# Kernel optimization log

Measured on AMD Instinct MI355X. Metric: run time of the kernel, lower is better.

The kernel has to match this reference:

```python
import jax, jax.numpy as jnp
import numpy as np

B, S, D, H = 4, 2048, 1024, 16
DH = D // H  # dim per head

def setup_inputs() -> dict:
    key = jax.random.key(0)
    ks = jax.random.split(key, 12)
    sc = 1.0 / np.sqrt(D)
    inp = {
        "key": jax.random.normal(ks[0], (B, S, D), jnp.float32),
        "value": jax.random.normal(ks[1], (B, S, D), jnp.float32),
        "query": jax.random.normal(ks[2], (B, S, D), jnp.float32),
        "mask": jax.random.randint(ks[3], (B, S, S), 0, 2).astype(bool),
        "Wq": jax.random.normal(ks[4], (D, D), jnp.float32) * sc,
        "bq": jnp.zeros((D,), jnp.float32),
        "Wk": jax.random.normal(ks[5], (D, D), jnp.float32) * sc,
        "bk": jnp.zeros((D,), jnp.float32),
        "Wv": jax.random.normal(ks[6], (D, D), jnp.float32) * sc,
        "bv": jnp.zeros((D,), jnp.float32),
        "Wo": jax.random.normal(ks[7], (D, D), jnp.float32) * sc,
        "bo": jnp.zeros((D,), jnp.float32),
    }
    return inp

def _shape(x, b):
    # [b, len, D] -> [b, H, len, DH]
    return x.reshape(b, -1, H, DH).transpose(0, 2, 1, 3)

def reference(key, value, query, mask, Wq, bq, Wk, bk, Wv, bv, Wo, bo):
    b = key.shape[0]
    q = _shape(query @ Wq.T + bq, b) / jnp.sqrt(jnp.asarray(DH, query.dtype))
    k = _shape(key @ Wk.T + bk, b)
    v = _shape(value @ Wv.T + bv, b)
    # scores: [b, H, q_len, k_len]
    scores = jnp.einsum("bhqd,bhkd->bhqk", q, k)
    scores = jnp.where(mask[:, None, :, :], jnp.asarray(-1e18, scores.dtype), scores)
    attn = jax.nn.softmax(scores, axis=-1)  # dropout is identity in eval mode
    ctx = jnp.einsum("bhqk,bhkd->bhqd", attn, v)
    ctx = ctx.transpose(0, 2, 1, 3).reshape(b, -1, H * DH)
    return ctx @ Wo.T + bo
```

## Files before the change

kernel.cpp:

```cpp
#include <hip/hip_runtime.h>

#define BB  4
#define SS  2048
#define DD  1024
#define HH  16
#define DHH 64
#define LOG2E 1.44269504088896340736f

typedef __attribute__((ext_vector_type(8)))  _Float16 half8;
typedef __attribute__((ext_vector_type(4)))  _Float16 half4;
typedef __attribute__((ext_vector_type(2)))  float    f32x2;
typedef __attribute__((ext_vector_type(4)))  float    f32x4;
typedef __attribute__((ext_vector_type(8)))  float    f32x8;
typedef __attribute__((ext_vector_type(16))) float    f32x16;
typedef __attribute__((ext_vector_type(4)))  unsigned int uint4v;

#if __has_builtin(__builtin_amdgcn_exp2f)
#define EXP2(x) __builtin_amdgcn_exp2f(x)
#else
#define EXP2(x) exp2f(x)
#endif

__device__ __forceinline__ void gload_lds16(const void* g, void* l) {
  __builtin_amdgcn_global_load_lds(
      (const __attribute__((address_space(1))) unsigned int*)g,
      (__attribute__((address_space(3))) unsigned int*)l, 16, 0, 0);
}

__device__ __forceinline__ void plswap(unsigned int& x, unsigned int& y) {
  auto r = __builtin_amdgcn_permlane32_swap(x, y, false, false);
  x = r[0]; y = r[1];
}
__device__ __forceinline__ float xhalf_sum(float v) {
  unsigned int x = __builtin_bit_cast(unsigned int, v), y = x;
  plswap(x, y);
  return __builtin_bit_cast(float, x) + __builtin_bit_cast(float, y);
}

__device__ __forceinline__ float tree16(f32x16 t) {
  f32x8 u = __builtin_shufflevector(t, t, 0, 1, 2, 3, 4, 5, 6, 7) +
            __builtin_shufflevector(t, t, 8, 9, 10, 11, 12, 13, 14, 15);
  f32x4 v = __builtin_shufflevector(u, u, 0, 1, 2, 3) +
            __builtin_shufflevector(u, u, 4, 5, 6, 7);
  f32x2 w2 = __builtin_shufflevector(v, v, 0, 1) + __builtin_shufflevector(v, v, 2, 3);
  return w2[0] + w2[1];
}

__global__ __launch_bounds__(256) void cvt_f32_f16(
    const float* __restrict__ in, _Float16* __restrict__ out, int n4) {
  int i = blockIdx.x * 256 + threadIdx.x;
  if (i >= n4) return;
  float4 a = reinterpret_cast<const float4*>(in)[i];
  half4 h;
  h[0] = (_Float16)a.x; h[1] = (_Float16)a.y;
  h[2] = (_Float16)a.z; h[3] = (_Float16)a.w;
  reinterpret_cast<half4*>(out)[i] = h;
}

__global__ __launch_bounds__(256) void cvt_in3(
    const float* __restrict__ s0, const float* __restrict__ s1,
    const float* __restrict__ s2,
    _Float16* __restrict__ d0, _Float16* __restrict__ d1,
    _Float16* __restrict__ d2, int n4) {
  int i = blockIdx.x * 256 + threadIdx.x;
  if (i >= n4) return;
  const float* s; _Float16* d;
  switch (blockIdx.y) {
    case 0: s = s0; d = d0; break;
    case 1: s = s1; d = d1; break;
    default: s = s2; d = d2; break;
  }
  float4 a = reinterpret_cast<const float4*>(s)[i];
  half4 h;
  h[0] = (_Float16)a.x; h[1] = (_Float16)a.y;
  h[2] = (_Float16)a.z; h[3] = (_Float16)a.w;
  reinterpret_cast<half4*>(d)[i] = h;
}

__global__ __launch_bounds__(256) void cvt_w4(
    const float* __restrict__ s0, const float* __restrict__ s1,
    const float* __restrict__ s2, const float* __restrict__ s3,
    _Float16* __restrict__ d0, _Float16* __restrict__ d1,
    _Float16* __restrict__ d2, _Float16* __restrict__ d3, int n4) {
  int i = blockIdx.x * 256 + threadIdx.x;
  if (i >= n4) return;
  const float* s; _Float16* d;
  switch (blockIdx.y) {
    case 0: s = s0; d = d0; break;
    case 1: s = s1; d = d1; break;
    case 2: s = s2; d = d2; break;
    default: s = s3; d = d3; break;
  }
  float4 a = reinterpret_cast<const float4*>(s)[i];
  half4 h;
  h[0] = (_Float16)a.x; h[1] = (_Float16)a.y;
  h[2] = (_Float16)a.z; h[3] = (_Float16)a.w;
  reinterpret_cast<half4*>(d)[i] = h;
}

__global__ __launch_bounds__(256) void pack_mask_kernel(
    const int* __restrict__ m, unsigned long long* __restrict__ bitsT) {
  size_t g = (size_t)blockIdx.x * 256 + threadIdx.x;
  unsigned long long bal = __ballot(m[g] != 0);
  if ((threadIdx.x & 63) == 0) {
    int key = (int)(g & (SS - 1));
    int q   = (int)((g >> 11) & (SS - 1));
    int b   = (int)(g >> 22);
    bitsT[((size_t)(b * (SS / 64) + (key >> 6))) * SS + q] = bal;
  }
}


#define GEMM_BODY(A, Bm, K)                                                       \
  __shared__ _Float16 lsA[128 * 64];                                              \
  __shared__ _Float16 lsB[128 * 64];                                              \
  const int t = threadIdx.x;                                                      \
  const int w = t >> 6, l = t & 63;                                               \
  const int l15 = l & 15, l4 = l >> 4;                                            \
  const int wm = (w >> 1) * 64, wn = (w & 1) * 64;                                \
  const int srow = l >> 3;                                                        \
  const int scolh = ((l & 7) ^ srow) * 8;                                         \
  f32x4 acc[4][4] = {};                                                           \
  const _Float16* gA = (A) + (size_t)(tm * 128) * (K);                            \
  const _Float16* gB = (Bm) + (size_t)(tn * 128) * (K);                           \
  for (int kt = 0; kt < (K); kt += 64) {                                          \
    _Pragma("unroll") for (int i = 0; i < 4; ++i) {                               \
      int c = w * 4 + i;                                                          \
      int row = c * 8 + srow;                                                     \
      gload_lds16(gA + (size_t)row * (K) + kt + scolh, lsA + c * 512);            \
      gload_lds16(gB + (size_t)row * (K) + kt + scolh, lsB + c * 512);            \
    }                                                                             \
    __syncthreads();                                                              \
    _Pragma("unroll") for (int kk = 0; kk < 2; ++kk) {                            \
      half8 aF[4], bF[4];                                                         \
      _Pragma("unroll") for (int x = 0; x < 4; ++x) {                             \
        int ra = wm + x * 16 + l15;                                               \
        aF[x] = *(const half8*)(lsA + ra * 64 + ((kk * 32 + l4 * 8) ^ ((ra & 7) * 8))); \
        int rb = wn + x * 16 + l15;                                               \
        bF[x] = *(const half8*)(lsB + rb * 64 + ((kk * 32 + l4 * 8) ^ ((rb & 7) * 8))); \
      }                                                                           \
      _Pragma("unroll") for (int x = 0; x < 4; ++x)                               \
        _Pragma("unroll") for (int y = 0; y < 4; ++y)                             \
          acc[x][y] = __builtin_amdgcn_mfma_f32_16x16x32_f16(aF[x], bF[y], acc[x][y], 0, 0, 0); \
    }                                                                             \
    __syncthreads();                                                              \
  }

template <int MODE>
__global__ __launch_bounds__(256, 2) void gemm_nt(
    const _Float16* __restrict__ A, const _Float16* __restrict__ Bm,
    const float* __restrict__ bias, void* __restrict__ out,
    int M, int N, int K, int tilesN) {
  const int nb8 = gridDim.x >> 3;
  const int bidx = (blockIdx.x & 7) * nb8 + (blockIdx.x >> 3);
  const int tm = bidx / tilesN, tn = bidx % tilesN;
  GEMM_BODY(A, Bm, K)
#pragma unroll
  for (int x = 0; x < 4; ++x) {
#pragma unroll
    for (int r = 0; r < 4; ++r) {
      int i = tm * 128 + wm + x * 16 + l4 * 4 + r;
#pragma unroll
      for (int y = 0; y < 4; ++y) {
        int j = tn * 128 + wn + y * 16 + l15;
        float v = acc[x][y][r];
        if (MODE == 0) {
          v = (v + bias[j]) * (0.125f * LOG2E);
          ((_Float16*)out)[(((size_t)(i >> 11) * HH + (j >> 6)) * SS + (i & (SS - 1))) * DHH + (j & 63)] =
              (_Float16)v;
        } else if (MODE == 1) {
          v = v + bias[j];
          ((_Float16*)out)[(((size_t)(i >> 11) * HH + (j >> 6)) * SS + (i & (SS - 1))) * DHH + (j & 63)] =
              (_Float16)v;
        } else if (MODE == 2) {
          v = v + bias[i];
          ((_Float16*)out)[((size_t)(j >> 11) * DD + i) * SS + (j & (SS - 1))] = (_Float16)v;
        } else {
          ((float*)out)[(size_t)i * N + j] = v + bias[j];
        }
      }
    }
  }
}

__global__ __launch_bounds__(256, 2) void gemm_qkv(
    const _Float16* __restrict__ xq, const _Float16* __restrict__ xk,
    const _Float16* __restrict__ xv,
    const _Float16* __restrict__ wq, const _Float16* __restrict__ wk,
    const _Float16* __restrict__ wv,
    const float* __restrict__ bq, const float* __restrict__ bk,
    const float* __restrict__ bv,
    _Float16* __restrict__ qh, _Float16* __restrict__ kh,
    _Float16* __restrict__ vt) {
  const int mode = blockIdx.y;
  const _Float16 *A, *Bm;
  const float* bias;
  int tilesN;
  if (mode == 0)      { A = xq; Bm = wq; bias = bq; tilesN = 8; }
  else if (mode == 1) { A = xk; Bm = wk; bias = bk; tilesN = 8; }
  else                { A = wv; Bm = xv; bias = bv; tilesN = 64; }

  const int bidx = (blockIdx.x & 7) * 64 + (blockIdx.x >> 3);
  const int tm = bidx / tilesN, tn = bidx % tilesN;
  GEMM_BODY(A, Bm, DD)
#pragma unroll
  for (int x = 0; x < 4; ++x) {
#pragma unroll
    for (int r = 0; r < 4; ++r) {
      int i = tm * 128 + wm + x * 16 + l4 * 4 + r;
#pragma unroll
      for (int y = 0; y < 4; ++y) {
        int j = tn * 128 + wn + y * 16 + l15;
        float v = acc[x][y][r];
        if (mode == 2) {
          v = v + bias[i];
          vt[((size_t)(j >> 11) * DD + i) * SS + (j & (SS - 1))] = (_Float16)v;
        } else {
          v = v + bias[j];
          if (mode == 0) v *= (0.125f * LOG2E);
          _Float16* o16 = mode ? kh : qh;
          o16[(((size_t)(i >> 11) * HH + (j >> 6)) * SS + (i & (SS - 1))) * DHH + (j & 63)] =
              (_Float16)v;
        }
      }
    }
  }
}

__global__ __launch_bounds__(256, 3) void attn_kernel(
    const _Float16* __restrict__ qh, const _Float16* __restrict__ kh,
    const _Float16* __restrict__ vt, const unsigned long long* __restrict__ mT,
    _Float16* __restrict__ ctx) {
  __shared__ _Float16 lsK[2][64 * 64];
  __shared__ _Float16 lsV[2][64 * 64];

  const int t = threadIdx.x;
  const int w = t >> 6, l = t & 63;
  const int l31 = l & 31, hi = l >> 5;
  const int srow = l >> 3;
  const int scolh = ((l & 7) ^ srow) * 8;

  const int bid = ((blockIdx.x & 7) << 7) | (blockIdx.x >> 3);
  const int bh = bid >> 4;
  const int qt = bid & 15;
  const int b = bh >> 4;
  const int h = bh & 15;
  const int qbase = qt * 128 + w * 32;

  const _Float16* qrow = qh + ((size_t)bh * SS + qbase + l31) * DHH + hi * 8;
  half8 bQ[4];
#pragma unroll
  for (int s = 0; s < 4; ++s) bQ[s] = *(const half8*)(qrow + s * 16);

  const _Float16* kbh = kh + (size_t)bh * SS * DHH;
  const _Float16* vbh = vt + (size_t)bh * DHH * SS;

  int boff[2][4];
  {
    const int swzb = (l31 & 7) * 16;
#pragma unroll
    for (int i = 0; i < 2; ++i)
#pragma unroll
      for (int s = 0; s < 4; ++s)
        boff[i][s] = (i * 32 + l31) * 128 + (((s * 16 + hi * 8) * 2) ^ swzb);
  }

  int ko0 = (w * 16 + srow) * DHH + scolh;
  int ko1 = ko0 + 8 * DHH;
  int vo0 = (w * 16 + srow) * SS + scolh;
  int vo1 = vo0 + 8 * SS;
  const int ldsc = (w * 2) * 512;

  f32x16 o0 = {}, o1 = {};
  float lsum = 0.f;

  const unsigned long long* mp = mT + (size_t)b * (SS / 64) * SS + qbase + l31;
  unsigned long long mb = mp[0];

  gload_lds16(kbh + ko0, &lsK[0][ldsc]);
  gload_lds16(kbh + ko1, &lsK[0][ldsc + 512]);
  gload_lds16(vbh + vo0, &lsV[0][ldsc]);
  gload_lds16(vbh + vo1, &lsV[0][ldsc + 512]);
  ko0 += 64 * DHH; ko1 += 64 * DHH; vo0 += 64; vo1 += 64;

#pragma unroll 2
  for (int kt = 0; kt < 32; ++kt) {
    const int cur = kt & 1;
    __syncthreads();
    if (kt < 31) {
      gload_lds16(kbh + ko0, &lsK[cur ^ 1][ldsc]);
      gload_lds16(kbh + ko1, &lsK[cur ^ 1][ldsc + 512]);
      gload_lds16(vbh + vo0, &lsV[cur ^ 1][ldsc]);
      gload_lds16(vbh + vo1, &lsV[cur ^ 1][ldsc + 512]);
      ko0 += 64 * DHH; ko1 += 64 * DHH; vo0 += 64; vo1 += 64;
    }
    unsigned long long mbn = 0;
    if (kt < 31) mbn = mp[(size_t)(kt + 1) * SS];

    const unsigned int mw0 = ((unsigned int)mb) >> (hi * 4);
    const unsigned int mw1 = ((unsigned int)(mb >> 32)) >> (hi * 4);
    const char* kbase = (const char*)(&lsK[0][0]) + cur * 8192;
    const char* vbase = (const char*)(&lsV[0][0]) + cur * 8192;

#pragma unroll
    for (int ns = 0; ns < 2; ++ns) {
      const unsigned int mwx = ns ? mw1 : mw0;
      f32x16 sc;
#pragma unroll
      for (int r = 0; r < 16; ++r) {
        const int p = (r & 3) + 8 * (r >> 2);
        int mneg = ((int)(mwx << (31 - p))) >> 31;
        sc[r] = __builtin_bit_cast(float, ((unsigned int)mneg) & 0xFF800000u);
      }
#pragma unroll
      for (int s = 0; s < 4; ++s) {
        half8 aK = *(const half8*)(kbase + boff[ns][s]);
        sc = __builtin_amdgcn_mfma_f32_32x32x16_f16(aK, bQ[s], sc, 0, 0, 0);
      }
#pragma unroll
      for (int r = 0; r < 16; ++r) sc[r] = EXP2(sc[r]);
      lsum += tree16(sc);
#pragma unroll
      for (int hf = 0; hf < 2; ++hf) {
        const int e = hf * 8;
        unsigned int pa = __builtin_bit_cast(unsigned int,
            __builtin_amdgcn_cvt_pkrtz(sc[e + 0], sc[e + 1]));
        unsigned int pb = __builtin_bit_cast(unsigned int,
            __builtin_amdgcn_cvt_pkrtz(sc[e + 2], sc[e + 3]));
        unsigned int pc = __builtin_bit_cast(unsigned int,
            __builtin_amdgcn_cvt_pkrtz(sc[e + 4], sc[e + 5]));
        unsigned int pd = __builtin_bit_cast(unsigned int,
            __builtin_amdgcn_cvt_pkrtz(sc[e + 6], sc[e + 7]));
        plswap(pa, pc);
        plswap(pb, pd);
        uint4v u4 = {pa, pb, pc, pd};
        half8 aP = __builtin_bit_cast(half8, u4);
        const int s = ns * 2 + hf;
        half8 bV0 = *(const half8*)(vbase + boff[0][s]);
        o0 = __builtin_amdgcn_mfma_f32_32x32x16_f16(aP, bV0, o0, 0, 0, 0);
        half8 bV1 = *(const half8*)(vbase + boff[1][s]);
        o1 = __builtin_amdgcn_mfma_f32_32x32x16_f16(aP, bV1, o1, 0, 0, 0);
      }
    }
    mb = mbn;
  }

  const float lrun = xhalf_sum(lsum);
  const float inv = 1.0f / lrun;
  _Float16* cbase = ctx + ((size_t)b * SS + qbase) * DD + h * DHH + l31;
#pragma unroll
  for (int r = 0; r < 16; ++r) {
    const int qr = (r & 3) + 8 * (r >> 2) + hi * 4;
    float ir = __shfl(inv, qr);
    cbase[(size_t)qr * DD]      = (_Float16)(o0[r] * ir);
    cbase[(size_t)qr * DD + 32] = (_Float16)(o1[r] * ir);
  }
}

extern "C" void kernel_launch(void* const* d_in, const int* in_sizes, int n_in,
                              void* d_out, int out_size, void* d_ws, size_t ws_size,
                              hipStream_t stream) {
  const float* key   = (const float*)d_in[0];
  const float* value = (const float*)d_in[1];
  const float* query = (const float*)d_in[2];
  const int*   mask  = (const int*)d_in[3];
  const float* Wq = (const float*)d_in[4];
  const float* bq = (const float*)d_in[5];
  const float* Wk = (const float*)d_in[6];
  const float* bk = (const float*)d_in[7];
  const float* Wv = (const float*)d_in[8];
  const float* bv = (const float*)d_in[9];
  const float* Wo = (const float*)d_in[10];
  const float* bo = (const float*)d_in[11];
  float* out = (float*)d_out;

  char* ws = (char*)d_ws;
  const int n4_in = BB * SS * DD / 4;
  const int n4_w  = DD * DD / 4;
  const size_t MB = 1048576;

  if (ws_size >= 106 * MB) {
    _Float16* xq = (_Float16*)(ws);
    _Float16* xk = (_Float16*)(ws + 16 * MB);
    _Float16* xv = (_Float16*)(ws + 32 * MB);
    _Float16* wq16 = (_Float16*)(ws + 48 * MB);
    _Float16* wk16 = (_Float16*)(ws + 50 * MB);
    _Float16* wv16 = (_Float16*)(ws + 52 * MB);
    _Float16* wo16 = (_Float16*)(ws + 54 * MB);
    _Float16* qh = (_Float16*)(ws + 56 * MB);
    _Float16* kh = (_Float16*)(ws + 72 * MB);
    _Float16* vt = (_Float16*)(ws + 88 * MB);
    unsigned long long* mbitsT = (unsigned long long*)(ws + 104 * MB);
    _Float16* ctx = xq;

    pack_mask_kernel<<<BB * SS * SS / 64 / 4, 256, 0, stream>>>(mask, mbitsT);
    cvt_w4<<<dim3(n4_w / 256, 4), 256, 0, stream>>>(Wq, Wk, Wv, Wo, wq16, wk16, wv16, wo16, n4_w);
    cvt_in3<<<dim3(n4_in / 256, 3), 256, 0, stream>>>(query, key, value, xq, xk, xv, n4_in);
    gemm_qkv<<<dim3(512, 3), 256, 0, stream>>>(xq, xk, xv, wq16, wk16, wv16,
                                               bq, bk, bv, qh, kh, vt);
    attn_kernel<<<BB * HH * (SS / 128), 256, 0, stream>>>(qh, kh, vt, mbitsT, ctx);
    gemm_nt<3><<<512, 256, 0, stream>>>(ctx, wo16, bo, out, BB * SS, DD, DD, DD / 128);
  } else {
    _Float16* x16  = (_Float16*)(ws);
    _Float16* wq16 = (_Float16*)(ws + 16777216);
    _Float16* wk16 = (_Float16*)(ws + 18874368);
    _Float16* wv16 = (_Float16*)(ws + 20971520);
    _Float16* wo16 = (_Float16*)(ws + 23068672);
    _Float16* qh   = (_Float16*)(ws + 25165824);
    _Float16* kh   = (_Float16*)(ws + 41943040);
    _Float16* vt   = (_Float16*)(ws + 58720256);
    unsigned long long* mbitsT = (unsigned long long*)(ws + 75497472);
    _Float16* ctx = x16;

    pack_mask_kernel<<<BB * SS * SS / 64 / 4, 256, 0, stream>>>(mask, mbitsT);
    cvt_w4<<<dim3(n4_w / 256, 4), 256, 0, stream>>>(Wq, Wk, Wv, Wo, wq16, wk16, wv16, wo16, n4_w);
    cvt_f32_f16<<<n4_in / 256, 256, 0, stream>>>(query, x16, n4_in);
    gemm_nt<0><<<512, 256, 0, stream>>>(x16, wq16, bq, qh, BB * SS, DD, DD, DD / 128);
    cvt_f32_f16<<<n4_in / 256, 256, 0, stream>>>(key, x16, n4_in);
    gemm_nt<1><<<512, 256, 0, stream>>>(x16, wk16, bk, kh, BB * SS, DD, DD, DD / 128);
    cvt_f32_f16<<<n4_in / 256, 256, 0, stream>>>(value, x16, n4_in);
    gemm_nt<2><<<512, 256, 0, stream>>>(wv16, x16, bv, vt, DD, BB * SS, DD, BB * SS / 128);
    attn_kernel<<<BB * HH * (SS / 128), 256, 0, stream>>>(qh, kh, vt, mbitsT, ctx);
    gemm_nt<3><<<512, 256, 0, stream>>>(ctx, wo16, bo, out, BB * SS, DD, DD, DD / 128);
  }
}
```

Before: 277.8 us.

## Split fused QKV GEMM into three launches and simplify attention LDS addressing

The fused three-mode QKV projection kernel is replaced by three separate templated GEMM launches, so each kernel's epilogue is specialised at compile time instead of branching on blockIdx.y. The attention kernel now computes LDS double-buffer addresses as byte offsets and its main loop unroll drops from 2 to 1, which is meant to cut register pressure and code size. The split gives up the larger single 1536-block grid and adds two extra kernel launches.

After: 263.8 us. -5.0%, faster.

```diff
diff --git a/kernel.cpp b/kernel.cpp
--- a/kernel.cpp
+++ b/kernel.cpp
@@ -183,50 +183,6 @@
   }
 }
 
-__global__ __launch_bounds__(256, 2) void gemm_qkv(
-    const _Float16* __restrict__ xq, const _Float16* __restrict__ xk,
-    const _Float16* __restrict__ xv,
-    const _Float16* __restrict__ wq, const _Float16* __restrict__ wk,
-    const _Float16* __restrict__ wv,
-    const float* __restrict__ bq, const float* __restrict__ bk,
-    const float* __restrict__ bv,
-    _Float16* __restrict__ qh, _Float16* __restrict__ kh,
-    _Float16* __restrict__ vt) {
-  const int mode = blockIdx.y;
-  const _Float16 *A, *Bm;
-  const float* bias;
-  int tilesN;
-  if (mode == 0)      { A = xq; Bm = wq; bias = bq; tilesN = 8; }
-  else if (mode == 1) { A = xk; Bm = wk; bias = bk; tilesN = 8; }
-  else                { A = wv; Bm = xv; bias = bv; tilesN = 64; }
-
-  const int bidx = (blockIdx.x & 7) * 64 + (blockIdx.x >> 3);
-  const int tm = bidx / tilesN, tn = bidx % tilesN;
-  GEMM_BODY(A, Bm, DD)
-#pragma unroll
-  for (int x = 0; x < 4; ++x) {
-#pragma unroll
-    for (int r = 0; r < 4; ++r) {
-      int i = tm * 128 + wm + x * 16 + l4 * 4 + r;
-#pragma unroll
-      for (int y = 0; y < 4; ++y) {
-        int j = tn * 128 + wn + y * 16 + l15;
-        float v = acc[x][y][r];
-        if (mode == 2) {
-          v = v + bias[i];
-          vt[((size_t)(j >> 11) * DD + i) * SS + (j & (SS - 1))] = (_Float16)v;
-        } else {
-          v = v + bias[j];
-          if (mode == 0) v *= (0.125f * LOG2E);
-          _Float16* o16 = mode ? kh : qh;
-          o16[(((size_t)(i >> 11) * HH + (j >> 6)) * SS + (i & (SS - 1))) * DHH + (j & 63)] =
-              (_Float16)v;
-        }
-      }
-    }
-  }
-}
-
 __global__ __launch_bounds__(256, 3) void attn_kernel(
     const _Float16* __restrict__ qh, const _Float16* __restrict__ kh,
     const _Float16* __restrict__ vt, const unsigned long long* __restrict__ mT,
@@ -269,7 +225,9 @@
   int ko1 = ko0 + 8 * DHH;
   int vo0 = (w * 16 + srow) * SS + scolh;
   int vo1 = vo0 + 8 * SS;
-  const int ldsc = (w * 2) * 512;
+  char* lsKb = (char*)&lsK[0][0];
+  char* lsVb = (char*)&lsV[0][0];
+  const int ldsb = w * 2048;
 
   f32x16 o0 = {}, o1 = {};
   float lsum = 0.f;
@@ -277,21 +235,22 @@
   const unsigned long long* mp = mT + (size_t)b * (SS / 64) * SS + qbase + l31;
   unsigned long long mb = mp[0];
 
-  gload_lds16(kbh + ko0, &lsK[0][ldsc]);
-  gload_lds16(kbh + ko1, &lsK[0][ldsc + 512]);
-  gload_lds16(vbh + vo0, &lsV[0][ldsc]);
-  gload_lds16(vbh + vo1, &lsV[0][ldsc + 512]);
+  gload_lds16(kbh + ko0, lsKb + ldsb);
+  gload_lds16(kbh + ko1, lsKb + ldsb + 1024);
+  gload_lds16(vbh + vo0, lsVb + ldsb);
+  gload_lds16(vbh + vo1, lsVb + ldsb + 1024);
   ko0 += 64 * DHH; ko1 += 64 * DHH; vo0 += 64; vo1 += 64;
 
-#pragma unroll 2
+#pragma unroll 1
   for (int kt = 0; kt < 32; ++kt) {
-    const int cur = kt & 1;
+    const int curb = (kt & 1) << 13;
+    const int othb = curb ^ 8192;
     __syncthreads();
     if (kt < 31) {
-      gload_lds16(kbh + ko0, &lsK[cur ^ 1][ldsc]);
-      gload_lds16(kbh + ko1, &lsK[cur ^ 1][ldsc + 512]);
-      gload_lds16(vbh + vo0, &lsV[cur ^ 1][ldsc]);
-      gload_lds16(vbh + vo1, &lsV[cur ^ 1][ldsc + 512]);
+      gload_lds16(kbh + ko0, lsKb + othb + ldsb);
+      gload_lds16(kbh + ko1, lsKb + othb + ldsb + 1024);
+      gload_lds16(vbh + vo0, lsVb + othb + ldsb);
+      gload_lds16(vbh + vo1, lsVb + othb + ldsb + 1024);
       ko0 += 64 * DHH; ko1 += 64 * DHH; vo0 += 64; vo1 += 64;
     }
     unsigned long long mbn = 0;
@@ -299,8 +258,8 @@
 
     const unsigned int mw0 = ((unsigned int)mb) >> (hi * 4);
     const unsigned int mw1 = ((unsigned int)(mb >> 32)) >> (hi * 4);
-    const char* kbase = (const char*)(&lsK[0][0]) + cur * 8192;
-    const char* vbase = (const char*)(&lsV[0][0]) + cur * 8192;
+    const char* kbase = lsKb + curb;
+    const char* vbase = lsVb + curb;
 
 #pragma unroll
     for (int ns = 0; ns < 2; ++ns) {
@@ -396,8 +355,9 @@
     pack_mask_kernel<<<BB * SS * SS / 64 / 4, 256, 0, stream>>>(mask, mbitsT);
     cvt_w4<<<dim3(n4_w / 256, 4), 256, 0, stream>>>(Wq, Wk, Wv, Wo, wq16, wk16, wv16, wo16, n4_w);
     cvt_in3<<<dim3(n4_in / 256, 3), 256, 0, stream>>>(query, key, value, xq, xk, xv, n4_in);
-    gemm_qkv<<<dim3(512, 3), 256, 0, stream>>>(xq, xk, xv, wq16, wk16, wv16,
-                                               bq, bk, bv, qh, kh, vt);
+    gemm_nt<0><<<512, 256, 0, stream>>>(xq, wq16, bq, qh, BB * SS, DD, DD, DD / 128);
+    gemm_nt<1><<<512, 256, 0, stream>>>(xk, wk16, bk, kh, BB * SS, DD, DD, DD / 128);
+    gemm_nt<2><<<512, 256, 0, stream>>>(wv16, xv, bv, vt, DD, BB * SS, DD, BB * SS / 128);
     attn_kernel<<<BB * HH * (SS / 128), 256, 0, stream>>>(qh, kh, vt, mbitsT, ctx);
     gemm_nt<3><<<512, 256, 0, stream>>>(ctx, wo16, bo, out, BB * SS, DD, DD, DD / 128);
   } else {
```
